# Kernel optimization log

Measured on AMD Instinct MI355X. Metric: run time of the kernel, lower is better.

Reference implementation:

```python
import jax, jax.numpy as jnp
import numpy as np

B, N, M, K = 8, 4096, 32, 72
D = 6 + K
W_REG, W_CLS = 3.0, 1.0
SIMOTA_Q = 4
IOU_LEN = 15.0
EPS = 1e-12
BIG = 100000.0


def setup_inputs() -> dict:
    key = jax.random.key(0)
    k1, k2, k3, k4, k5, k6 = jax.random.split(key, 6)
    preds = jax.random.normal(k1, (B, N, D), jnp.float32)
    # pred x-offsets in pixel range
    preds = preds.at[..., 6:].set(jax.random.uniform(k2, (B, N, K), jnp.float32, 0.0, 800.0))
    tgt = jax.random.normal(k3, (B, M, D), jnp.float32) * 0.1
    tgt = tgt.at[..., 1].set(jax.random.randint(k4, (B, M), 0, 2).astype(jnp.float32))
    tgt = tgt.at[..., 2:5].set(jax.random.uniform(k5, (B, M, 3), jnp.float32) * jnp.array([800.0, 320.0, 3.14159], jnp.float32))
    # target x-offsets, some out-of-range -> invalid points
    tgt = tgt.at[..., 6:].set(jax.random.uniform(k6, (B, M, K), jnp.float32, -50.0, 850.0))
    masks = jax.random.uniform(jax.random.fold_in(key, 7), (B, M)) > 0.2
    return {"preds": preds, "targets": tgt, "masks": masks, "img_w": 800, "img_h": 320}


def _focal_cost(cls_logits, gt_labels, alpha=0.25, gamma=2.0):
    # cls_logits [B,N,2], gt_labels [B,M] int -> [B,N,M]
    p = jax.nn.sigmoid(cls_logits)
    neg = -jnp.log(1.0 - p + EPS) * (1.0 - alpha) * p ** gamma
    pos = -jnp.log(p + EPS) * alpha * (1.0 - p) ** gamma
    diff = pos - neg  # [B,N,2]
    idx = jnp.broadcast_to(gt_labels[:, None, :], (gt_labels.shape[0], cls_logits.shape[1], gt_labels.shape[1]))
    return jnp.take_along_axis(diff, idx, axis=2)


def _pairwise_line_iou(pred_x, tgt_x, img_w, length=IOU_LEN):
    # pred_x [B,N,K], tgt_x [B,M,K] -> [B,N,M]
    p = pred_x[:, :, None, :]
    t = tgt_x[:, None, :, :]
    ovr = jnp.minimum(p + length, t + length) - jnp.maximum(p - length, t - length)
    union = jnp.maximum(p + length, t + length) - jnp.minimum(p - length, t - length)
    invalid = (t < 0) | (t >= img_w)
    ovr = jnp.where(invalid, 0.0, ovr)
    union = jnp.where(invalid, 0.0, union)
    return ovr.sum(-1) / (union.sum(-1) + 1e-9)


def _cost(preds, targets, masks, img_w):
    # -> cost [B,N,M]
    pred_dx = preds[..., 6:]
    tgt_dx = targets[..., 6:]
    invalid = (tgt_dx < 0) | (tgt_dx >= img_w)  # [B,M,K]
    lengths = jnp.maximum((~invalid).sum(-1), 1)  # [B,M]
    d = jnp.abs(tgt_dx[:, None, :, :] - pred_dx[:, :, None, :])  # [B,N,M,K]
    d = jnp.where(invalid[:, None, :, :], 0.0, d)
    distances = d.sum(-1) / lengths[:, None, :].astype(preds.dtype)  # [B,N,M]
    max_d = jnp.maximum(distances.max(axis=(1, 2), keepdims=True), 1e-6)
    dist_s = 1.0 - distances / max_d + 0.01
    xy = jnp.linalg.norm(preds[:, :, None, 2:4] - targets[:, None, :, 2:4], axis=-1)
    xy_s = 1.0 - xy / jnp.maximum(xy.max(axis=(1, 2), keepdims=True), 1e-6) + 0.01
    th = jnp.abs(preds[:, :, None, 4] - targets[:, None, :, 4])
    th_s = 1.0 - th / jnp.maximum(th.max(axis=(1, 2), keepdims=True), 1e-6) + 0.01
    cls_cost = _focal_cost(preds[..., :2], targets[..., 1].astype(jnp.int32))
    cost = -((dist_s * xy_s * th_s) ** 2) * W_REG + cls_cost * W_CLS
    return jnp.where(masks[:, None, :], cost, BIG)


def _assign(cost, iou, masks):
    b, n, m = cost.shape
    ious = jnp.where(masks[:, None, :], iou, 0.0)
    ious = jnp.maximum(ious, 0.0)
    n_cand = min(SIMOTA_Q, n)
    topk_ious, _ = jax.lax.top_k(jnp.swapaxes(ious, 1, 2), n_cand)  # [B,M,q]
    dynamic_ks = jnp.clip(topk_ious.sum(-1).astype(jnp.int32), 1, n)  # [B,M]
    # since line-iou <= 1, dynamic_ks <= SIMOTA_Q -> static max_k = n_cand
    max_k = n_cand
    _, topk_idx = jax.lax.top_k(-jnp.swapaxes(cost, 1, 2), max_k)  # [B,M,max_k] smallest costs
    k_mask = jnp.arange(max_k)[None, None, :] < dynamic_ks[:, :, None]  # [B,M,max_k]
    bi = jnp.arange(b)[:, None, None]
    mi = jnp.arange(m)[None, :, None]
    mmT = jnp.zeros((b, m, n), cost.dtype).at[bi, mi, topk_idx].set(k_mask.astype(cost.dtype))
    matching = jnp.swapaxes(mmT, 1, 2)  # [B,N,M]
    matching = jnp.where(masks[:, None, :], matching, 0.0)
    matched_gt = matching.sum(-1)  # [B,N]
    conflict = matched_gt > 1.0
    cost_inf = jnp.where(matching == 0.0, jnp.inf, cost)
    min_idx = jnp.argmin(cost_inf, axis=2)  # [B,N]
    one_hot = jax.nn.one_hot(min_idx, m, dtype=cost.dtype)
    matching = jnp.where(conflict[:, :, None], one_hot, matching)
    assigned = matching.sum(-1) > 0.0
    matched_t = jnp.argmax(matching, axis=2)
    matched_t = jnp.where(assigned, matched_t, -1)
    return assigned, matched_t


def reference(preds, targets, masks, img_w, img_h):
    cost = _cost(preds, targets, masks, img_w)
    iou = _pairwise_line_iou(preds[..., 6:], targets[..., 6:], img_w)
    return _assign(cost, iou, masks)
```

## Files before the change

kernel.cpp:

```cpp
#include <hip/hip_runtime.h>
#include <stdint.h>

#define BB 8
#define NN 4096
#define MM 32
#define KK 72
#define DD 78
#define PAD 76

static constexpr float EPSF = 1e-12f;

__device__ inline bool getmask(const void* masks, int flag, int i) {
  if (flag) return ((const unsigned char*)masks)[i] != 0;
  return ((const int*)masks)[i] != 0;
}

__device__ inline unsigned long long packkey(float c, int m) {
  unsigned u = __float_as_uint(c);
  unsigned k = ((int)u < 0) ? ~u : (u ^ 0x80000000u);
  return ((unsigned long long)k << 32) | (unsigned)m;
}

__global__ __launch_bounds__(128) void k_pairs(
    const float* __restrict__ preds, const float* __restrict__ tgts,
    const int* __restrict__ imgw_p, const unsigned char* __restrict__ masks_raw,
    float* __restrict__ sadA, float4* __restrict__ pc4, float* __restrict__ cls,
    float* __restrict__ part, unsigned* __restrict__ mmask,
    unsigned long long* __restrict__ cmin, int* __restrict__ flag) {
  __shared__ __align__(16) float t_xs[MM][PAD];
  __shared__ __align__(16) float am_s[MM][PAD];
  __shared__ __align__(16) float px_s[64][PAD];
  __shared__ float pc_s[64][4];
  __shared__ float t_cx[MM], t_cy[MM], t_th[MM], t_len[MM];
  __shared__ float redv[2][3];

  const int b = blockIdx.x >> 6;
  const int n0 = (blockIdx.x & 63) << 6;
  const int tid = threadIdx.x;
  const float imgw = (float)(*imgw_p);

  if (tid < 64) {
    mmask[blockIdx.x * 64 + tid] = 0u;
    cmin[blockIdx.x * 64 + tid] = ~0ull;
  }
  if (blockIdx.x == 0 && tid < 64) {
    int i = tid * 4;
    bool nz = false;
#pragma unroll
    for (int j = 1; j < 4; ++j)
      if (masks_raw[i + j] != 0) nz = true;
    unsigned long long bal = __ballot(nz);
    if (tid == 0) *flag = (bal != 0ull) ? 1 : 0;
  }

  for (int idx = tid; idx < MM * DD; idx += 128) {
    int m = idx / DD, j = idx - m * DD;
    float v = tgts[((size_t)b * MM + m) * DD + j];
    if (j >= 6) {
      t_xs[m][j - 6] = v;
      am_s[m][j - 6] = (v >= 0.0f && v < imgw) ? 1.0f : 0.0f;
    } else if (j == 2) t_cx[m] = v;
    else if (j == 3) t_cy[m] = v;
    else if (j == 4) t_th[m] = v;
  }
  for (int idx = tid; idx < 64 * KK; idx += 128) {
    int ni = idx / KK, k = idx - ni * KK;
    px_s[ni][k] = preds[((size_t)b * NN + (n0 + ni)) * DD + 6 + k];
  }
  for (int idx = tid; idx < 64 * 3; idx += 128) {
    int ni = idx / 3, c = idx - ni * 3;
    pc_s[ni][c] = preds[((size_t)b * NN + (n0 + ni)) * DD + 2 + c];
  }
  {
    int ni = tid >> 1, c = tid & 1;
    float lg = preds[((size_t)b * NN + (n0 + ni)) * DD + c];
    float pp = 1.0f / (1.0f + expf(-lg));
    float neg = -logf(1.0f - pp + EPSF) * 0.75f * (pp * pp);
    float pos = -logf(pp + EPSF) * 0.25f * ((1.0f - pp) * (1.0f - pp));
    cls[((size_t)b * NN + (n0 + ni)) * 2 + c] = pos - neg;
  }
  __syncthreads();
  if (tid < 64)
    pc4[(size_t)b * NN + n0 + tid] =
        make_float4(pc_s[tid][0], pc_s[tid][1], pc_s[tid][2], 0.0f);
  if (tid < MM) {
    float V = 0.f;
    for (int k = 0; k < KK; ++k) V += am_s[tid][k];
    t_len[tid] = (V > 0.f) ? V : 1.0f;
  }
  __syncthreads();

  const int mt = tid >> 4;
  const int nt = tid & 15;
  const int mbase = mt << 2;

  const float4* t0r = reinterpret_cast<const float4*>(&t_xs[mbase + 0][0]);
  const float4* t1r = reinterpret_cast<const float4*>(&t_xs[mbase + 1][0]);
  const float4* t2r = reinterpret_cast<const float4*>(&t_xs[mbase + 2][0]);
  const float4* t3r = reinterpret_cast<const float4*>(&t_xs[mbase + 3][0]);
  const float4* a0r = reinterpret_cast<const float4*>(&am_s[mbase + 0][0]);
  const float4* a1r = reinterpret_cast<const float4*>(&am_s[mbase + 1][0]);
  const float4* a2r = reinterpret_cast<const float4*>(&am_s[mbase + 2][0]);
  const float4* a3r = reinterpret_cast<const float4*>(&am_s[mbase + 3][0]);
  const float4* p0r = reinterpret_cast<const float4*>(&px_s[nt][0]);
  const float4* p1r = reinterpret_cast<const float4*>(&px_s[nt + 16][0]);
  const float4* p2r = reinterpret_cast<const float4*>(&px_s[nt + 32][0]);
  const float4* p3r = reinterpret_cast<const float4*>(&px_s[nt + 48][0]);

  float s00 = 0.f, s01 = 0.f, s02 = 0.f, s03 = 0.f;
  float s10 = 0.f, s11 = 0.f, s12 = 0.f, s13 = 0.f;
  float s20 = 0.f, s21 = 0.f, s22 = 0.f, s23 = 0.f;
  float s30 = 0.f, s31 = 0.f, s32 = 0.f, s33 = 0.f;

#define ST(S, T, A, P)                       \
  S = fmaf(fabsf((T).x - (P).x), (A).x, S);  \
  S = fmaf(fabsf((T).y - (P).y), (A).y, S);  \
  S = fmaf(fabsf((T).z - (P).z), (A).z, S);  \
  S = fmaf(fabsf((T).w - (P).w), (A).w, S);
#pragma unroll 3
  for (int q = 0; q < KK / 4; ++q) {
    float4 T0 = t0r[q], A0 = a0r[q], T1 = t1r[q], A1 = a1r[q];
    float4 T2 = t2r[q], A2 = a2r[q], T3 = t3r[q], A3 = a3r[q];
    float4 P0 = p0r[q], P1 = p1r[q], P2 = p2r[q], P3 = p3r[q];
    ST(s00, T0, A0, P0) ST(s01, T0, A0, P1) ST(s02, T0, A0, P2) ST(s03, T0, A0, P3)
    ST(s10, T1, A1, P0) ST(s11, T1, A1, P1) ST(s12, T1, A1, P2) ST(s13, T1, A1, P3)
    ST(s20, T2, A2, P0) ST(s21, T2, A2, P1) ST(s22, T2, A2, P2) ST(s23, T2, A2, P3)
    ST(s30, T3, A3, P0) ST(s31, T3, A3, P1) ST(s32, T3, A3, P2) ST(s33, T3, A3, P3)
  }
#undef ST

  float md = 0.f, mxy = 0.f, mth = 0.f;
#define FIN(S, MI, NJ)                                                        \
  {                                                                           \
    float sad = S;                                                            \
    int mi = mbase + (MI);                                                    \
    int nr = nt + 16 * (NJ);                                                  \
    float dval = sad / t_len[mi];                  \
    float dx = pc_s[nr][0] - t_cx[mi], dy = pc_s[nr][1] - t_cy[mi];           \
    float xyv = sqrtf(fmaf(dx, dx, dy * dy));  \
    float thv = fabsf(pc_s[nr][2] - t_th[mi]);                                \
    sadA[((size_t)(b * MM + mi)) * NN + n0 + nr] = sad;                       \
    md = fmaxf(md, dval); mxy = fmaxf(mxy, xyv); mth = fmaxf(mth, thv);       \
  }
  FIN(s00, 0, 0) FIN(s01, 0, 1) FIN(s02, 0, 2) FIN(s03, 0, 3)
  FIN(s10, 1, 0) FIN(s11, 1, 1) FIN(s12, 1, 2) FIN(s13, 1, 3)
  FIN(s20, 2, 0) FIN(s21, 2, 1) FIN(s22, 2, 2) FIN(s23, 2, 3)
  FIN(s30, 3, 0) FIN(s31, 3, 1) FIN(s32, 3, 2) FIN(s33, 3, 3)
#undef FIN

  for (int off = 32; off; off >>= 1) {
    md = fmaxf(md, __shfl_down(md, off));
    mxy = fmaxf(mxy, __shfl_down(mxy, off));
    mth = fmaxf(mth, __shfl_down(mth, off));
  }
  if ((tid & 63) == 0) {
    int w = tid >> 6;
    redv[w][0] = md; redv[w][1] = mxy; redv[w][2] = mth;
  }
  __syncthreads();
  if (tid == 0) {
    part[(size_t)blockIdx.x * 3 + 0] = fmaxf(redv[0][0], redv[1][0]);
    part[(size_t)blockIdx.x * 3 + 1] = fmaxf(redv[0][1], redv[1][1]);
    part[(size_t)blockIdx.x * 3 + 2] = fmaxf(redv[0][2], redv[1][2]);
  }
}

__global__ __launch_bounds__(1024) void k_assign(
    const float* __restrict__ sadA, const float4* __restrict__ pc4,
    const float* __restrict__ cls, const float* __restrict__ tgts,
    const int* __restrict__ imgw_p, const float* __restrict__ part,
    const void* __restrict__ masks, const int* __restrict__ flag,
    unsigned* __restrict__ mmask, unsigned long long* __restrict__ cmin) {
  const int b = blockIdx.x >> 5;
  const int m = blockIdx.x & 31;
  if (!getmask(masks, *flag, b * MM + m)) return;

  const int tid = threadIdx.x;
  __shared__ float bcast[3];
  __shared__ float scal[8];

  if (tid < 192) {
    int g = tid >> 6, e = tid & 63;
    float v = part[((size_t)(b * 64 + e)) * 3 + g];
    for (int off = 32; off; off >>= 1) v = fmaxf(v, __shfl_down(v, off));
    if ((tid & 63) == 0) bcast[g] = v;
  }
  if (tid >= 896 && tid < 960) {
    int lane = tid - 896;
    const float* trow = tgts + ((size_t)(b * MM + m)) * DD;
    const float imgw = (float)(*imgw_p);
    float t0 = trow[6 + lane];
    int c = (t0 >= 0.0f && t0 < imgw) ? 1 : 0;
    if (lane < KK - 64) {
      float t1 = trow[6 + 64 + lane];
      c += (t1 >= 0.0f && t1 < imgw) ? 1 : 0;
    }
    for (int off = 32; off; off >>= 1) c += __shfl_down(c, off);
    if (lane == 0) {
      float V = (float)c;
      scal[3] = (V > 0.f) ? V : 1.0f;
      scal[4] = 30.0f * V;
    }
  }
  if (tid == 1023) {
    const float* trow = tgts + ((size_t)(b * MM + m)) * DD;
    scal[0] = trow[2]; scal[1] = trow[3]; scal[2] = trow[4];
  }
  __syncthreads();

  const float maxd = fmaxf(bcast[0], 1e-6f);
  const float maxxy = fmaxf(bcast[1], 1e-6f);
  const float maxth = fmaxf(bcast[2], 1e-6f);
  const float tcx = scal[0], tcy = scal[1], tth = scal[2];
  const float len = scal[3], v30 = scal[4];
  const int label = (int)tgts[((size_t)b * MM + m) * DD + 1];

  const int n0 = tid << 2;
  float4 s4 = *reinterpret_cast<const float4*>(sadA + ((size_t)(b * MM + m)) * NN + n0);
  const float4* pcb = pc4 + (size_t)b * NN + n0;
  float4 q0 = pcb[0], q1 = pcb[1], q2 = pcb[2], q3 = pcb[3];
  const float4* cbase = reinterpret_cast<const float4*>(cls + ((size_t)b * NN + n0) * 2);
  float4 c0 = cbase[0], c1 = cbase[1];

  float se[4] = {s4.x, s4.y, s4.z, s4.w};
  float cxe[4] = {q0.x, q1.x, q2.x, q3.x};
  float cye[4] = {q0.y, q1.y, q2.y, q3.y};
  float the[4] = {q0.z, q1.z, q2.z, q3.z};
  float clv[4] = {label ? c0.y : c0.x, label ? c0.w : c0.z,
                  label ? c1.y : c1.x, label ? c1.w : c1.z};

  float cc[4]; int ci[4]; float vv[4];
#pragma unroll
  for (int e = 0; e < 4; ++e) {
    float sad = se[e];
    float dval = sad / len;
    float dx = cxe[e] - tcx, dy = cye[e] - tcy;
    float xyv = sqrtf(fmaf(dx, dx, dy * dy));
    float thv = fabsf(the[e] - tth);
    float iv = (v30 - sad) / ((v30 + sad) + 1e-9f);
    float ds = (1.0f - dval / maxd) + 0.01f;
    float xs = (1.0f - xyv / maxxy) + 0.01f;
    float ts = (1.0f - thv / maxth) + 0.01f;
    float r = (ds * xs) * ts;
    cc[e] = -(r * r) * 3.0f + clv[e] * 1.0f;
    ci[e] = n0 + e;
    vv[e] = fmaxf(iv, 0.0f);
  }

  __shared__ float ls_c[64];  __shared__ int ls_ci[64];
  __shared__ float ls_v[64];  __shared__ int ls_vi[64];

  const int wid = tid >> 6, lane = tid & 63;
  unsigned usedC = 0, usedV = 0;
  float wcv[4]; int wci[4]; float wvv[4]; int wvi[4];

#pragma unroll
  for (int r = 0; r < 4; ++r) {
    float bv = 3e38f; int bi = 0x7fffffff; int be = -1;
#pragma unroll
    for (int e = 0; e < 4; ++e)
      if (!((usedC >> e) & 1) && (cc[e] < bv || (cc[e] == bv && ci[e] < bi))) {
        bv = cc[e]; bi = ci[e]; be = e;
      }
    float v = bv; int i = bi;
#pragma unroll
    for (int off = 32; off; off >>= 1) {
      float ov = __shfl_xor(v, off); int oi = __shfl_xor(i, off);
      if (ov < v || (ov == v && oi < i)) { v = ov; i = oi; }
    }
    if (be >= 0 && i == bi) usedC |= 1u << be;
    wcv[r] = v; wci[r] = i;

    float bw = -1.0f; int bj = 0x7fffffff; int bf = -1;
#pragma unroll
    for (int e = 0; e < 4; ++e)
      if (!((usedV >> e) & 1) && (vv[e] > bw || (vv[e] == bw && ci[e] < bj))) {
        bw = vv[e]; bj = ci[e]; bf = e;
      }
    float w = bw; int j = bj;
#pragma unroll
    for (int off = 32; off; off >>= 1) {
      float ow = __shfl_xor(w, off); int oj = __shfl_xor(j, off);
      if (ow > w || (ow == w && oj < j)) { w = ow; j = oj; }
    }
    if (bf >= 0 && j == bj) usedV |= 1u << bf;
    wvv[r] = w; wvi[r] = j;
  }

  if (lane == 0) {
#pragma unroll
    for (int r = 0; r < 4; ++r) {
      ls_c[wid * 4 + r] = wcv[r]; ls_ci[wid * 4 + r] = wci[r];
      ls_v[wid * 4 + r] = wvv[r]; ls_vi[wid * 4 + r] = wvi[r];
    }
  }
  __syncthreads();

  if (tid < 64) {
    float c = ls_c[tid]; int i = ls_ci[tid];
    float w = ls_v[tid]; int j = ls_vi[tid];
    int gidx[4]; float gcst[4]; float gsum = 0.0f;
#pragma unroll
    for (int r = 0; r < 4; ++r) {
      float v = c; int vi = i;
#pragma unroll
      for (int off = 32; off; off >>= 1) {
        float ov = __shfl_xor(v, off); int oi = __shfl_xor(vi, off);
        if (ov < v || (ov == v && oi < vi)) { v = ov; vi = oi; }
      }
      if (i == vi) c = 3e38f;
      gidx[r] = vi; gcst[r] = v;

      float u = w; int ui = j;
#pragma unroll
      for (int off = 32; off; off >>= 1) {
        float ou = __shfl_xor(u, off); int oi = __shfl_xor(ui, off);
        if (ou > u || (ou == u && oi < ui)) { u = ou; ui = oi; }
      }
      if (j == ui) w = -1.0f;
      gsum += u;
    }
    if (tid == 0) {
      int k = (int)gsum;
      if (k < 1) k = 1;
      if (k > 4) k = 4;
      for (int s = 0; s < k; ++s) {
        atomicOr(&mmask[(size_t)b * NN + gidx[s]], 1u << m);
        atomicMin(&cmin[(size_t)b * NN + gidx[s]], packkey(gcst[s], m));
      }
    }
  }
}

__global__ __launch_bounds__(256) void k_final(
    const unsigned* __restrict__ mmask,
    const unsigned long long* __restrict__ cmin, int* __restrict__ out) {
  int idx = blockIdx.x * 256 + threadIdx.x;
  if (idx >= BB * NN) return;
  unsigned mm = mmask[idx];
  int pc = __popc(mm);
  int t = pc ? (int)(unsigned)(cmin[idx] & 0xFFFFFFFFull) : -1;
  out[idx] = pc ? 1 : 0;
  out[BB * NN + idx] = t;
}

extern "C" void kernel_launch(void* const* d_in, const int* in_sizes, int n_in,
                              void* d_out, int out_size, void* d_ws, size_t ws_size,
                              hipStream_t stream) {
  const float* preds = (const float*)d_in[0];
  const float* tgts = (const float*)d_in[1];
  const void* masks = d_in[2];
  const int* imgw = (const int*)d_in[3];

  char* ws = (char*)d_ws;
  float* sadA = (float*)ws;
  char* p = ws + (size_t)BB * MM * NN * sizeof(float);
  float4* pc4 = (float4*)p;
  p += (size_t)BB * NN * sizeof(float4);
  float* cls = (float*)p;
  p += (size_t)BB * NN * 2 * sizeof(float);
  float* part = (float*)p;
  p += (size_t)1024 * 3 * sizeof(float);
  unsigned* mmask = (unsigned*)p;
  p += (size_t)BB * NN * sizeof(unsigned);
  unsigned long long* cmin = (unsigned long long*)p;
  p += (size_t)BB * NN * sizeof(unsigned long long);
  int* flag = (int*)p;

  k_pairs<<<dim3(BB * 64), dim3(128), 0, stream>>>(
      preds, tgts, imgw, (const unsigned char*)masks,
      sadA, pc4, cls, part, mmask, cmin, flag);
  k_assign<<<dim3(BB * MM), dim3(1024), 0, stream>>>(
      sadA, pc4, cls, tgts, imgw, part, masks, flag, mmask, cmin);
  k_final<<<dim3((BB * NN + 255) / 256), dim3(256), 0, stream>>>(
      mmask, cmin, (int*)d_out);
}
```

Measured before the change: 49.42 us.

## Double k_pairs block size and compute validity mask on the fly

k_pairs now runs 256 threads per block, and each thread computes a 2x4 tile of pair sums instead of 4x4. This halves the accumulator registers per thread and increases parallelism. The shared-memory validity-mask array is removed; the mask is recomputed from target x values inside the inner loop, which cuts LDS traffic and footprint but adds compare/select work per element. The reduction and staging loops are adjusted for four wavefronts.

```diff
diff --git a/kernel.cpp b/kernel.cpp
--- a/kernel.cpp
+++ b/kernel.cpp
@@ -21,18 +21,17 @@
   return ((unsigned long long)k << 32) | (unsigned)m;
 }
 
-__global__ __launch_bounds__(128) void k_pairs(
+__global__ __launch_bounds__(256) void k_pairs(
     const float* __restrict__ preds, const float* __restrict__ tgts,
     const int* __restrict__ imgw_p, const unsigned char* __restrict__ masks_raw,
     float* __restrict__ sadA, float4* __restrict__ pc4, float* __restrict__ cls,
     float* __restrict__ part, unsigned* __restrict__ mmask,
     unsigned long long* __restrict__ cmin, int* __restrict__ flag) {
   __shared__ __align__(16) float t_xs[MM][PAD];
-  __shared__ __align__(16) float am_s[MM][PAD];
   __shared__ __align__(16) float px_s[64][PAD];
   __shared__ float pc_s[64][4];
   __shared__ float t_cx[MM], t_cy[MM], t_th[MM], t_len[MM];
-  __shared__ float redv[2][3];
+  __shared__ float redv[4][3];
 
   const int b = blockIdx.x >> 6;
   const int n0 = (blockIdx.x & 63) << 6;
@@ -53,25 +52,23 @@
     if (tid == 0) *flag = (bal != 0ull) ? 1 : 0;
   }
 
-  for (int idx = tid; idx < MM * DD; idx += 128) {
+  for (int idx = tid; idx < MM * DD; idx += 256) {
     int m = idx / DD, j = idx - m * DD;
     float v = tgts[((size_t)b * MM + m) * DD + j];
-    if (j >= 6) {
-      t_xs[m][j - 6] = v;
-      am_s[m][j - 6] = (v >= 0.0f && v < imgw) ? 1.0f : 0.0f;
-    } else if (j == 2) t_cx[m] = v;
+    if (j >= 6) t_xs[m][j - 6] = v;
+    else if (j == 2) t_cx[m] = v;
     else if (j == 3) t_cy[m] = v;
     else if (j == 4) t_th[m] = v;
   }
-  for (int idx = tid; idx < 64 * KK; idx += 128) {
+  for (int idx = tid; idx < 64 * KK; idx += 256) {
     int ni = idx / KK, k = idx - ni * KK;
     px_s[ni][k] = preds[((size_t)b * NN + (n0 + ni)) * DD + 6 + k];
   }
-  for (int idx = tid; idx < 64 * 3; idx += 128) {
-    int ni = idx / 3, c = idx - ni * 3;
+  if (tid < 192) {
+    int ni = tid / 3, c = tid - ni * 3;
     pc_s[ni][c] = preds[((size_t)b * NN + (n0 + ni)) * DD + 2 + c];
   }
-  {
+  if (tid < 128) {
     int ni = tid >> 1, c = tid & 1;
     float lg = preds[((size_t)b * NN + (n0 + ni)) * DD + c];
     float pp = 1.0f / (1.0f + expf(-lg));
@@ -84,24 +81,21 @@
     pc4[(size_t)b * NN + n0 + tid] =
         make_float4(pc_s[tid][0], pc_s[tid][1], pc_s[tid][2], 0.0f);
   if (tid < MM) {
-    float V = 0.f;
-    for (int k = 0; k < KK; ++k) V += am_s[tid][k];
-    t_len[tid] = (V > 0.f) ? V : 1.0f;
+    int V = 0;
+    for (int k = 0; k < KK; ++k) {
+      float t = t_xs[tid][k];
+      if (t >= 0.0f && t < imgw) V++;
+    }
+    t_len[tid] = (float)(V > 0 ? V : 1);
   }
   __syncthreads();
 
   const int mt = tid >> 4;
   const int nt = tid & 15;
-  const int mbase = mt << 2;
+  const int mbase = mt << 1;
 
   const float4* t0r = reinterpret_cast<const float4*>(&t_xs[mbase + 0][0]);
   const float4* t1r = reinterpret_cast<const float4*>(&t_xs[mbase + 1][0]);
-  const float4* t2r = reinterpret_cast<const float4*>(&t_xs[mbase + 2][0]);
-  const float4* t3r = reinterpret_cast<const float4*>(&t_xs[mbase + 3][0]);
-  const float4* a0r = reinterpret_cast<const float4*>(&am_s[mbase + 0][0]);
-  const float4* a1r = reinterpret_cast<const float4*>(&am_s[mbase + 1][0]);
-  const float4* a2r = reinterpret_cast<const float4*>(&am_s[mbase + 2][0]);
-  const float4* a3r = reinterpret_cast<const float4*>(&am_s[mbase + 3][0]);
   const float4* p0r = reinterpret_cast<const float4*>(&px_s[nt][0]);
   const float4* p1r = reinterpret_cast<const float4*>(&px_s[nt + 16][0]);
   const float4* p2r = reinterpret_cast<const float4*>(&px_s[nt + 32][0]);
@@ -109,25 +103,27 @@
 
   float s00 = 0.f, s01 = 0.f, s02 = 0.f, s03 = 0.f;
   float s10 = 0.f, s11 = 0.f, s12 = 0.f, s13 = 0.f;
-  float s20 = 0.f, s21 = 0.f, s22 = 0.f, s23 = 0.f;
-  float s30 = 0.f, s31 = 0.f, s32 = 0.f, s33 = 0.f;
-
+
+#define MSK(T) \
+  make_float4(((T).x >= 0.0f && (T).x < imgw) ? 1.0f : 0.0f, \
+              ((T).y >= 0.0f && (T).y < imgw) ? 1.0f : 0.0f, \
+              ((T).z >= 0.0f && (T).z < imgw) ? 1.0f : 0.0f, \
+              ((T).w >= 0.0f && (T).w < imgw) ? 1.0f : 0.0f)
 #define ST(S, T, A, P)                       \
   S = fmaf(fabsf((T).x - (P).x), (A).x, S);  \
   S = fmaf(fabsf((T).y - (P).y), (A).y, S);  \
   S = fmaf(fabsf((T).z - (P).z), (A).z, S);  \
   S = fmaf(fabsf((T).w - (P).w), (A).w, S);
-#pragma unroll 3
+#pragma unroll 6
   for (int q = 0; q < KK / 4; ++q) {
-    float4 T0 = t0r[q], A0 = a0r[q], T1 = t1r[q], A1 = a1r[q];
-    float4 T2 = t2r[q], A2 = a2r[q], T3 = t3r[q], A3 = a3r[q];
+    float4 T0 = t0r[q], T1 = t1r[q];
+    float4 A0 = MSK(T0), A1 = MSK(T1);
     float4 P0 = p0r[q], P1 = p1r[q], P2 = p2r[q], P3 = p3r[q];
     ST(s00, T0, A0, P0) ST(s01, T0, A0, P1) ST(s02, T0, A0, P2) ST(s03, T0, A0, P3)
     ST(s10, T1, A1, P0) ST(s11, T1, A1, P1) ST(s12, T1, A1, P2) ST(s13, T1, A1, P3)
-    ST(s20, T2, A2, P0) ST(s21, T2, A2, P1) ST(s22, T2, A2, P2) ST(s23, T2, A2, P3)
-    ST(s30, T3, A3, P0) ST(s31, T3, A3, P1) ST(s32, T3, A3, P2) ST(s33, T3, A3, P3)
   }
 #undef ST
+#undef MSK
 
   float md = 0.f, mxy = 0.f, mth = 0.f;
 #define FIN(S, MI, NJ)                                                        \
@@ -144,8 +140,6 @@
   }
   FIN(s00, 0, 0) FIN(s01, 0, 1) FIN(s02, 0, 2) FIN(s03, 0, 3)
   FIN(s10, 1, 0) FIN(s11, 1, 1) FIN(s12, 1, 2) FIN(s13, 1, 3)
-  FIN(s20, 2, 0) FIN(s21, 2, 1) FIN(s22, 2, 2) FIN(s23, 2, 3)
-  FIN(s30, 3, 0) FIN(s31, 3, 1) FIN(s32, 3, 2) FIN(s33, 3, 3)
 #undef FIN
 
   for (int off = 32; off; off >>= 1) {
@@ -159,9 +153,12 @@
   }
   __syncthreads();
   if (tid == 0) {
-    part[(size_t)blockIdx.x * 3 + 0] = fmaxf(redv[0][0], redv[1][0]);
-    part[(size_t)blockIdx.x * 3 + 1] = fmaxf(redv[0][1], redv[1][1]);
-    part[(size_t)blockIdx.x * 3 + 2] = fmaxf(redv[0][2], redv[1][2]);
+    float a0 = fmaxf(fmaxf(redv[0][0], redv[1][0]), fmaxf(redv[2][0], redv[3][0]));
+    float a1 = fmaxf(fmaxf(redv[0][1], redv[1][1]), fmaxf(redv[2][1], redv[3][1]));
+    float a2 = fmaxf(fmaxf(redv[0][2], redv[1][2]), fmaxf(redv[2][2], redv[3][2]));
+    part[(size_t)blockIdx.x * 3 + 0] = a0;
+    part[(size_t)blockIdx.x * 3 + 1] = a1;
+    part[(size_t)blockIdx.x * 3 + 2] = a2;
   }
 }
 
@@ -367,7 +364,7 @@
   p += (size_t)BB * NN * sizeof(unsigned long long);
   int* flag = (int*)p;
 
-  k_pairs<<<dim3(BB * 64), dim3(128), 0, stream>>>(
+  k_pairs<<<dim3(BB * 64), dim3(256), 0, stream>>>(
       preds, tgts, imgw, (const unsigned char*)masks,
       sadA, pc4, cls, part, mmask, cmin, flag);
   k_assign<<<dim3(BB * MM), dim3(1024), 0, stream>>>(
```

New measurement: 40.81 us (median of 2 runs). 17.4% less time.
